# Kernel optimization log

Measured on AMD Instinct MI355X. Metric: run time of the kernel, lower is better.

Reference implementation:

```python
import jax, jax.numpy as jnp
import numpy as np
from jax import lax
import math

B, C, H, W = 2, 128, 128, 256
K = 3
KK = K * K
AUX = C + 5

def conv2d(x, w, b, pad):
    out = lax.conv_general_dilated(x, w, (1, 1), [(pad, pad), (pad, pad)],
                                   dimension_numbers=('NCHW', 'OIHW', 'NCHW'))
    return out + b[None, :, None, None]

def erp_coord(h, w):
    xs = jnp.linspace(-math.pi, math.pi, w)
    ys = jnp.linspace(-math.pi / 2, math.pi / 2, h)
    theta = jnp.broadcast_to(xs[None, :], (h, w))
    phi = jnp.broadcast_to(ys[:, None], (h, w))
    return jnp.stack([jnp.sin(theta), jnp.cos(theta), jnp.sin(phi), jnp.cos(phi)], 0)[None]

def freq_energy(x, h, w):
    mag = jnp.abs(jnp.fft.rfft2(x, norm='ortho')).mean(1, keepdims=True)
    # bilinear resize (align_corners=False, half-pixel) to (h, w)
    return jax.image.resize(mag, (x.shape[0], 1, h, w), method='linear', antialias=False)

def deform_sample(x, offset):
    # x: (b,c,H,W); offset: (b, 2*KK, H, W)
    b, c, h, w = x.shape
    off = offset.reshape(b, KK, 2, h, w)
    xx = jnp.arange(w, dtype=x.dtype)[None, None, None, :]
    yy = jnp.arange(h, dtype=x.dtype)[None, None, :, None]
    # align_corners=True normalize/unnormalize cancels exactly
    px = xx + off[:, :, 0]  # (b,KK,h,w)
    py = yy + off[:, :, 1]
    x0 = jnp.floor(px).astype(jnp.int32); x1 = x0 + 1
    y0 = jnp.floor(py).astype(jnp.int32); y1 = y0 + 1
    wx1 = px - x0.astype(x.dtype); wx0 = 1.0 - wx1
    wy1 = py - y0.astype(x.dtype); wy0 = 1.0 - wy1
    flat = x.reshape(b, c, h * w)

    def gather(ix, iy):
        valid = ((ix >= 0) & (ix < w) & (iy >= 0) & (iy < h)).astype(x.dtype)
        idx = jnp.clip(iy, 0, h - 1) * w + jnp.clip(ix, 0, w - 1)  # (b,KK,h,w)
        g = jax.vmap(lambda f, i: f[:, i])(flat, idx)  # (b,c,KK,h,w)
        return g * valid[:, None]

    out = (gather(x0, y0) * (wx0 * wy0)[:, None]
           + gather(x1, y0) * (wx1 * wy0)[:, None]
           + gather(x0, y1) * (wx0 * wy1)[:, None]
           + gather(x1, y1) * (wx1 * wy1)[:, None])
    return out.reshape(b, c * KK, h, w)

def setup_inputs() -> dict:
    key = jax.random.key(0)
    ks = jax.random.split(key, 12)
    s = lambda *sh: 1.0 / np.sqrt(np.prod(sh[1:]))
    def unif(k, *sh):
        return jax.random.uniform(k, sh, jnp.float32, -s(*sh), s(*sh))
    return {
        'x': jax.random.normal(ks[0], (B, C, H, W), jnp.float32),
        'offset_w': unif(ks[1], 2 * KK, AUX, 3, 3),
        'offset_b': jnp.zeros((2 * KK,), jnp.float32),
        'gate_w1': unif(ks[2], AUX // 2, AUX, 3, 3),
        'gate_b1': jnp.zeros((AUX // 2,), jnp.float32),
        'gate_w2': unif(ks[3], 1, AUX // 2, 1, 1),
        'gate_b2': jnp.zeros((1,), jnp.float32),
        'base_w': unif(ks[4], C, C, K, K),
        'base_b': jnp.zeros((C,), jnp.float32),
        'def_w': jax.random.normal(ks[5], (C, C, K, K), jnp.float32) * s(C, C, K, K),
        'def_b': jnp.zeros((C,), jnp.float32),
    }

def reference(x, offset_w, offset_b, gate_w1, gate_b1, gate_w2, gate_b2,
              base_w, base_b, def_w, def_b):
    b, c, h, w = x.shape
    coord = jnp.broadcast_to(erp_coord(h, w), (b, 4, h, w)).astype(x.dtype)
    fe = freq_energy(x, h, w)
    aux = jnp.concatenate([x, coord, fe], 1)
    offset = conv2d(aux, offset_w, offset_b, 1)
    g = jax.nn.relu(conv2d(aux, gate_w1, gate_b1, 1))
    gate = jax.nn.sigmoid(conv2d(g, gate_w2, gate_b2, 0))
    y_base = conv2d(x, base_w, base_b, K // 2)
    sampled = deform_sample(x, offset)  # (b, c*KK, h, w)
    y_def = conv2d(sampled, def_w.reshape(c, c * KK, 1, 1), def_b, 0)
    return (1.0 - gate) * y_base + gate * y_def
```

## Files before the change

kernel.cpp:

```cpp
#include <hip/hip_runtime.h>
#include <hip/hip_bf16.h>

#define BB 2
#define CC 128
#define HH 128
#define WW 256
#define HWs (HH*WW)
#define PI_F 3.14159265358979323846f

typedef __attribute__((ext_vector_type(8))) short bf16x8;
typedef __attribute__((ext_vector_type(8))) unsigned short u16x8;
typedef __attribute__((ext_vector_type(4))) float f32x4;
typedef __attribute__((ext_vector_type(2))) float f32x2;

__device__ __forceinline__ ushort f2bf(float f) {
  uint u = __float_as_uint(f);
  u = (u + 0x7fffu + ((u >> 16) & 1u)) >> 16;
  return (ushort)u;
}
__device__ __forceinline__ float bf2f(ushort u) {
  return __uint_as_float(((uint)u) << 16);
}
__device__ __forceinline__ uint comb4(uint u0, uint u1, uint u2, uint u3,
                                      f32x2 g0, f32x2 g1, f32x2 g2, f32x2 g3) {
  f32x2 a0 = (f32x2){__uint_as_float(u0 << 16), __uint_as_float(u0 & 0xffff0000u)};
  f32x2 a1 = (f32x2){__uint_as_float(u1 << 16), __uint_as_float(u1 & 0xffff0000u)};
  f32x2 a2 = (f32x2){__uint_as_float(u2 << 16), __uint_as_float(u2 & 0xffff0000u)};
  f32x2 a3 = (f32x2){__uint_as_float(u3 << 16), __uint_as_float(u3 & 0xffff0000u)};
  f32x2 s = a0 * g0 + a1 * g1 + a2 * g2 + a3 * g3;
  uint ua = __float_as_uint(s.x) + 0x8000u;
  uint ub = __float_as_uint(s.y) + 0x8000u;
  return (ua >> 16) | (ub & 0xffff0000u);
}

__global__ __launch_bounds__(256) void prep_kernel(
    const float* __restrict__ bw, const float* __restrict__ dw,
    const float* __restrict__ ow, const float* __restrict__ gw,
    const float* __restrict__ x,
    ushort* __restrict__ apkF, ushort* __restrict__ apkA,
    ushort* __restrict__ a1, ushort* __restrict__ a2,
    ushort* __restrict__ xt) {
  __shared__ ushort sT[64][128];
  int bid = blockIdx.x;
  int tid = threadIdx.x;
  if (bid >= 284) {
    int blk = bid - 284;
    int wt = blk & 3, h = (blk >> 2) & 127, b = blk >> 9;
    int t = tid;
    const float* xb = x + ((size_t)b * CC * HH + h) * WW;
    ushort* ob = xt + (((size_t)b * HH + h) * WW) * 128;
    {
      int w = t & 63;
      int sw = (w & 7) << 3;
#pragma unroll
      for (int it = 0; it < 4; ++it) {
        int oct = (t >> 6) + it * 4;
        u16x8 v;
#pragma unroll
        for (int j = 0; j < 8; ++j)
          v[j] = f2bf(xb[(size_t)(oct * 8 + j) * HWs + wt * 64 + w]);
        *(u16x8*)&sT[w][(oct << 3) ^ sw] = v;
      }
    }
    __syncthreads();
#pragma unroll
    for (int it = 0; it < 4; ++it) {
      int u = t + it * 256;
      int w = u >> 4, oct = u & 15;
      u16x8 v = *(const u16x8*)&sT[w][(oct << 3) ^ ((w & 7) << 3)];
      *(u16x8*)&ob[(size_t)(wt * 64 + w) * 128 + oct * 8] = v;
    }
    return;
  }
  if (bid < 144) {
    int gid = bid * 256 + tid;
    int lane = gid & 63;
    int kf = (gid >> 6) & 3;
    int mf = (gid >> 8) & 7;
    int chunk = gid >> 11;
    int part = chunk >= 9;
    int tap = part ? chunk - 9 : chunk;
    int m = mf * 16 + (lane & 15);
    int cb = kf * 32 + ((lane >> 4) << 3);
    const float* src = part ? dw : bw;
    ushort* dst = apkF + (size_t)gid * 8;
#pragma unroll
    for (int j = 0; j < 8; ++j)
      dst[j] = f2bf(src[(size_t)m * 1152 + (size_t)(cb + j) * 9 + tap]);
  } else if (bid < 212) {
    int gid = (bid - 144) * 256 + tid;
    if (gid >= 17280) return;
    int lane = gid & 63;
    int kf = (gid >> 6) % 5;
    int mf = (gid / 320) % 6;
    int tap = gid / 1920;
    int m = mf * 16 + (lane & 15);
    int cb = kf * 32 + ((lane >> 4) << 3);
#pragma unroll
    for (int j = 0; j < 8; ++j) {
      int c = cb + j;
      float v = 0.f;
      if (c < 133) {
        if (m < 18) v = ow[(size_t)m * 1197 + c * 9 + tap];
        else if (m < 84) v = gw[(size_t)(m - 18) * 1197 + c * 9 + tap];
      }
      apkA[(size_t)gid * 8 + j] = f2bf(v);
    }
  } else {
    int gid = (bid - 212) * 256 + tid;
    if (gid < 10240) {
      int lane = gid & 63, kf = (gid >> 6) & 7, mf = gid >> 9;
      int m = mf * 16 + (lane & 15);
      int kk0 = kf * 32 + ((lane >> 4) << 3);
#pragma unroll
      for (int j = 0; j < 8; ++j) {
        int kk = kk0 + j;
        float v = 0.f;
        if (m < 129)      { int tt = (m * kk) & 255;         v =  cosf(tt * (PI_F / 128.f)); }
        else if (m < 258) { int tt = ((m - 129) * kk) & 255; v = -sinf(tt * (PI_F / 128.f)); }
        a1[(size_t)gid * 8 + j] = f2bf(v);
      }
    } else if (gid < 18432) {
      int q = gid - 10240;
      int lane = q & 63, kf = (q >> 6) & 7, mf = q >> 9;
      int m = mf * 16 + (lane & 15);
      int g = m & 127;
      int kk0 = kf * 32 + ((lane >> 4) << 3);
#pragma unroll
      for (int j = 0; j < 8; ++j) {
        int kk = kk0 + j;
        int h2 = kk & 127;
        int tt = (g * h2) & 127;
        float ang = tt * (PI_F / 64.f);
        float v = (m < 128) ? ((kk < 128) ? cosf(ang) : sinf(ang))
                            : ((kk < 128) ? -sinf(ang) : cosf(ang));
        a2[(size_t)q * 8 + j] = f2bf(v);
      }
    }
  }
}

__global__ __launch_bounds__(256) void dft1_kernel(const float* __restrict__ x,
    const ushort* __restrict__ a1pk, ushort* __restrict__ F1) {
  int bid = blockIdx.x;
  int bc = bid >> 1, nh = bid & 1;
  int t = threadIdx.x, lane = t & 63, wv = t >> 6;
  int q8 = (lane >> 4) << 3, rq = (lane >> 4) << 2;
  const bf16x8* APK = (const bf16x8*)a1pk;
  ushort* f1b = F1 + (size_t)bc * 36864;
  f32x4 acc[5][4];
#pragma unroll
  for (int i = 0; i < 5; ++i)
#pragma unroll
    for (int n = 0; n < 4; ++n) acc[i][n] = (f32x4){0.f, 0.f, 0.f, 0.f};
  for (int kf = 0; kf < 8; ++kf) {
    bf16x8 av[5];
#pragma unroll
    for (int i = 0; i < 5; ++i)
      av[i] = APK[(size_t)((wv * 5 + i) * 8 + kf) * 64 + lane];
#pragma unroll
    for (int n2 = 0; n2 < 4; ++n2) {
      int nf = nh * 4 + n2;
      int hh = nf * 16 + (lane & 15);
      const float* xp = x + (((size_t)bc * HH + hh) << 8) + kf * 32 + q8;
      float4 xa = *(const float4*)xp;
      float4 xb4 = *(const float4*)(xp + 4);
      bf16x8 bv;
      bv[0] = (short)f2bf(xa.x); bv[1] = (short)f2bf(xa.y);
      bv[2] = (short)f2bf(xa.z); bv[3] = (short)f2bf(xa.w);
      bv[4] = (short)f2bf(xb4.x); bv[5] = (short)f2bf(xb4.y);
      bv[6] = (short)f2bf(xb4.z); bv[7] = (short)f2bf(xb4.w);
#pragma unroll
      for (int i = 0; i < 5; ++i)
        acc[i][n2] = __builtin_amdgcn_mfma_f32_16x16x32_bf16(av[i], bv, acc[i][n2], 0, 0, 0);
    }
  }
#pragma unroll
  for (int n2 = 0; n2 < 4; ++n2) {
    int hh = (nh * 4 + n2) * 16 + (lane & 15);
#pragma unroll
    for (int i = 0; i < 5; ++i) {
#pragma unroll
      for (int r = 0; r < 4; ++r) {
        int m = (wv * 5 + i) * 16 + rq + r;
        if (m < 258) {
          int sel = m >= 129;
          int k = sel ? m - 129 : m;
          f1b[(size_t)k * 256 + sel * 128 + hh] = f2bf(acc[i][n2][r]);
        }
      }
    }
  }
}

__global__ __launch_bounds__(256) void dft2_kernel(const ushort* __restrict__ F1,
    const ushort* __restrict__ a2pk, float* __restrict__ magbuf) {
  int bid = blockIdx.x;
  int bc = bid / 3, ng = bid % 3;
  int t = threadIdx.x, lane = t & 63, wv = t >> 6;
  int q8 = (lane >> 4) << 3, rq = (lane >> 4) << 2;
  const bf16x8* APK = (const bf16x8*)a2pk;
  const ushort* f1b = F1 + (size_t)bc * 36864;
  float* mb = magbuf + (size_t)bc * 18432;
  f32x4 acc[4][3];
#pragma unroll
  for (int i = 0; i < 4; ++i)
#pragma unroll
    for (int n = 0; n < 3; ++n) acc[i][n] = (f32x4){0.f, 0.f, 0.f, 0.f};
  for (int kf = 0; kf < 8; ++kf) {
    bf16x8 av[4];
#pragma unroll
    for (int i = 0; i < 4; ++i) {
      int mf = (i < 2) ? (2 * wv + i) : (2 * wv + (i - 2) + 8);
      av[i] = APK[(size_t)(mf * 8 + kf) * 64 + lane];
    }
#pragma unroll
    for (int n2 = 0; n2 < 3; ++n2) {
      int nf = ng * 3 + n2;
      int krow = nf * 16 + (lane & 15);
      bf16x8 bv = *(const bf16x8*)&f1b[(size_t)krow * 256 + kf * 32 + q8];
#pragma unroll
      for (int i = 0; i < 4; ++i)
        acc[i][n2] = __builtin_amdgcn_mfma_f32_16x16x32_bf16(av[i], bv, acc[i][n2], 0, 0, 0);
    }
  }
#pragma unroll
  for (int n2 = 0; n2 < 3; ++n2) {
    int k = (ng * 3 + n2) * 16 + (lane & 15);
    if (k < 129) {
#pragma unroll
      for (int pr = 0; pr < 2; ++pr) {
#pragma unroll
        for (int r = 0; r < 4; ++r) {
          int g = (2 * wv + pr) * 16 + rq + r;
          float vr = acc[pr][n2][r], vi = acc[pr + 2][n2][r];
          mb[(size_t)g * 144 + k] = sqrtf(vr * vr + vi * vi);
        }
      }
    }
  }
}

__global__ __launch_bounds__(256) void fe_reduce_kernel(const float* __restrict__ magbuf,
    float* __restrict__ fe) {
  int bid = blockIdx.x;
  int i = (bid >> 3) * 256 + threadIdx.x;
  int cq = bid & 7;
  if (i >= 36864) return;
  int k = i % 144;
  int gb = i / 144;
  int g = gb & 127, b = gb >> 7;
  if (k >= 129) return;
  const float* mp = magbuf + (size_t)b * 128 * 18432 + (size_t)g * 144 + k
                  + (size_t)cq * 16 * 18432;
  float s = 0.f;
#pragma unroll
  for (int c = 0; c < 16; ++c) s += mp[(size_t)c * 18432];
  atomicAdd(&fe[((size_t)b * 128 + g) * 129 + k],
            s * (1.0f / (181.01933598375618f * 128.0f)));
}

__global__ __launch_bounds__(256) void aux_conv_kernel(
    const ushort* __restrict__ xt, const float* __restrict__ fe,
    const ushort* __restrict__ apk,
    const float* __restrict__ offset_b, const float* __restrict__ gate_b1,
    const float* __restrict__ w2, const float* __restrict__ b2,
    float* __restrict__ offs, float* __restrict__ gate) {
  __shared__ ushort Win3[3 * 68 * 64];
  __shared__ ushort coordS[204 * 8];
  __shared__ float gldP[64][8];
  int t = threadIdx.x;
  int bid = blockIdx.x;
  int lin = (bid & 7) * 128 + (bid >> 3);
  int bz = lin >> 9;
  int rest = lin & 511;
  int h = rest >> 2, w0 = (rest & 3) << 6;
  int lane = t & 63, wid = t >> 6;
  int wm = wid >> 1, wn = wid & 1;
  int l15 = lane & 15, lg = lane >> 4;
  int rq = lg << 2;
  const bf16x8* APK = (const bf16x8*)apk;
  const ushort* xtb = xt + (size_t)bz * 4194304;
  const bf16x8 zvb = (bf16x8){0, 0, 0, 0, 0, 0, 0, 0};

  if (t < 204) {
    int r = t / 68, c = t - r * 68;
    int gy = h - 1 + r, gx = w0 - 2 + c;
    u16x8 v = (u16x8){0, 0, 0, 0, 0, 0, 0, 0};
    if ((unsigned)gy < 128u && (unsigned)gx < 256u) {
      float th = -PI_F + (float)gx * (2.0f * PI_F / 255.0f);
      float ph = -0.5f * PI_F + (float)gy * (PI_F / 127.0f);
      float sxc = ((float)gx + 0.5f) * (129.0f / 256.0f) - 0.5f;
      float fx = floorf(sxc);
      int x0 = (int)fx;
      float fr = sxc - fx;
      int x1 = min(x0 + 1, 128);
      x0 = max(x0, 0);
      const float* fb = fe + ((size_t)bz * 128 + gy) * 129;
      float fv = fb[x0] * (1.f - fr) + fb[x1] * fr;
      v[0] = f2bf(sinf(th)); v[1] = f2bf(cosf(th));
      v[2] = f2bf(sinf(ph)); v[3] = f2bf(cosf(ph));
      v[4] = f2bf(fv);
    }
    *(u16x8*)&coordS[t * 8] = v;
  }

  f32x4 acc[3][2];
#pragma unroll
  for (int i = 0; i < 3; ++i) {
    acc[i][0] = (f32x4){0.f, 0.f, 0.f, 0.f};
    acc[i][1] = (f32x4){0.f, 0.f, 0.f, 0.f};
  }
  int p0 = wn * 32 + l15, p1 = p0 + 16;

  for (int half = 0; half < 2; ++half) {
    if (half) __syncthreads();
    for (int it = 0; it < 7; ++it) {
      int u = it * 256 + t;
      if (u < 1632) {
        int s = u & 7;
        int c = (u >> 3) % 68;
        int r = u / 544;
        int gy = h - 1 + r, gx = w0 - 2 + c;
        u16x8 v = (u16x8){0, 0, 0, 0, 0, 0, 0, 0};
        if ((unsigned)gy < 128u && (unsigned)gx < 256u)
          v = *(const u16x8*)&xtb[((((size_t)gy << 8) + gx) << 7) + (half << 6) + (s << 3)];
        *(u16x8*)&Win3[((r * 68 + c) << 6) + ((s ^ (c & 7)) << 3)] = v;
      }
    }
    __syncthreads();

    for (int tap = 0; tap < 9; ++tap) {
      int ky = tap / 3 - 1, kx = tap % 3 - 1;
      int rr = ky + 1;
      int c0 = p0 + kx + 2, c1 = p1 + kx + 2;
      int nkf = half ? 3 : 2;
      for (int kfi = 0; kfi < nkf; ++kfi) {
        bf16x8 b0, b1;
        int kf;
        if (kfi < 2) {
          kf = half * 2 + kfi;
          int s = kfi * 4 + lg;
          b0 = *(const bf16x8*)&Win3[((rr * 68 + c0) << 6) + ((s ^ (c0 & 7)) << 3)];
          b1 = *(const bf16x8*)&Win3[((rr * 68 + c1) << 6) + ((s ^ (c1 & 7)) << 3)];
        } else {
          kf = 4;
          b0 = (lg == 0) ? *(const bf16x8*)&coordS[(rr * 68 + c0) * 8] : zvb;
          b1 = (lg == 0) ? *(const bf16x8*)&coordS[(rr * 68 + c1) * 8] : zvb;
        }
        int fb = (tap * 6 + wm * 3) * 5 + kf;
#pragma unroll
        for (int mfi = 0; mfi < 3; ++mfi) {
          bf16x8 av = APK[(size_t)(fb + mfi * 5) * 64 + lane];
          acc[mfi][0] = __builtin_amdgcn_mfma_f32_16x16x32_bf16(av, b0, acc[mfi][0], 0, 0, 0);
          acc[mfi][1] = __builtin_amdgcn_mfma_f32_16x16x32_bf16(av, b1, acc[mfi][1], 0, 0, 0);
        }
      }
    }
  }

  float gp[2] = {0.f, 0.f};
#pragma unroll
  for (int nf = 0; nf < 2; ++nf) {
    int p = wn * 32 + nf * 16 + l15;
    int w = w0 + p;
#pragma unroll
    for (int mfi = 0; mfi < 3; ++mfi) {
#pragma unroll
      for (int r = 0; r < 4; ++r) {
        int oc = wm * 48 + mfi * 16 + rq + r;
        float v = acc[mfi][nf][r];
        if (oc < 18) {
          offs[((size_t)bz * 18 + oc) * HWs + h * WW + w] = v + offset_b[oc];
        } else if (oc < 84) {
          gp[nf] += w2[oc - 18] * fmaxf(v + gate_b1[oc - 18], 0.f);
        }
      }
    }
  }
  gldP[p0][wm * 4 + lg] = gp[0];
  gldP[p1][wm * 4 + lg] = gp[1];
  __syncthreads();
  if (t < 64) {
    float s = b2[0];
#pragma unroll
    for (int i = 0; i < 8; ++i) s += gldP[t][i];
    gate[(size_t)bz * HWs + h * WW + w0 + t] = 1.f / (1.f + expf(-s));
  }
}

__global__ __launch_bounds__(256) void fused_out_kernel(
    const ushort* __restrict__ xt, const float* __restrict__ offsp,
    const ushort* __restrict__ apk,
    const float* __restrict__ base_b, const float* __restrict__ def_b,
    const float* __restrict__ gate, float* __restrict__ out) {
  __shared__ ushort Win[4 * 68 * 64];
  __shared__ ushort Bt[2][64][64];
  __shared__ float gvS[64];
  __shared__ float bbS[128], bdS[128];
  int t = threadIdx.x;
  int bid = blockIdx.x;
  int lin = (bid & 7) * 128 + (bid >> 3);
  int bz = lin >> 9;
  int rest = lin & 511;
  int h = rest >> 2, w0 = (rest & 3) << 6;
  int lane = t & 63, wv = t >> 6;
  int l15 = lane & 15, lg = lane >> 4;
  int rq = lg << 2;
  const ushort* xtb = xt + (size_t)bz * 4194304;
  const bf16x8* APK = (const bf16x8*)apk;
  const u16x8 zv = (u16x8){0, 0, 0, 0, 0, 0, 0, 0};

  if (t < 64) gvS[t] = gate[(size_t)bz * HWs + h * WW + w0 + t];
  else if (t < 192) {
    int c = t - 64;
    bbS[c] = base_b[c];
    bdS[c] = def_b[c];
  }

  int p = t & 63, o4 = t >> 6;
  int mw = w0 + p;
  float oxr[9], oyr[9];
#pragma unroll
  for (int d = 0; d < 9; ++d) {
    oxr[d] = offsp[((size_t)bz * 18 + 2 * d) * HWs + h * WW + mw];
    oyr[d] = offsp[((size_t)bz * 18 + 2 * d + 1) * HWs + h * WW + mw];
  }

  f32x4 accB[2][4], accD[2][4];
#pragma unroll
  for (int mi = 0; mi < 2; ++mi)
#pragma unroll
    for (int nf = 0; nf < 4; ++nf) {
      accB[mi][nf] = (f32x4){0.f, 0.f, 0.f, 0.f};
      accD[mi][nf] = (f32x4){0.f, 0.f, 0.f, 0.f};
    }

  for (int half = 0; half < 2; ++half) {
#pragma unroll
    for (int it = 0; it < 9; ++it) {
      int u = it * 256 + t;
      if (u < 2176) {
        int s = u & 7;
        int c = (u >> 3) % 68;
        int r = u / 544;
        int gy = h - 1 + r, gx = w0 - 2 + c;
        u16x8 v = zv;
        if ((unsigned)gy < 128u && (unsigned)gx < 256u)
          v = *(const u16x8*)&xtb[((((size_t)gy << 8) + gx) << 7) + (half << 6) + (s << 3)];
        *(u16x8*)&Win[((r * 68 + c) << 6) + ((s ^ (c & 7)) << 3)] = v;
      }
    }
    __syncthreads();

    auto stage = [&](int nb, int d) {
      float px = (float)mw + oxr[d], py = (float)h + oyr[d];
      float fx = floorf(px), fy = floorf(py);
      int x0 = (int)fx, y0 = (int)fy;
      float wx1 = px - fx, wy1 = py - fy;
      float wx0 = 1.f - wx1, wy0 = 1.f - wy1;
      int x1 = x0 + 1, y1 = y0 + 1;
      bool vx0 = (unsigned)x0 < 256u, vx1 = (unsigned)x1 < 256u;
      bool vy0 = (unsigned)y0 < 128u, vy1 = (unsigned)y1 < 128u;
      float g0 = (vx0 && vy0) ? wx0 * wy0 : 0.f;
      float g1 = (vx1 && vy0) ? wx1 * wy0 : 0.f;
      float g2 = (vx0 && vy1) ? wx0 * wy1 : 0.f;
      float g3 = (vx1 && vy1) ? wx1 * wy1 : 0.f;
      f32x2 G0 = (f32x2){g0, g0}, G1 = (f32x2){g1, g1};
      f32x2 G2 = (f32x2){g2, g2}, G3 = (f32x2){g3, g3};
      int cx0 = min(max(x0, 0), 255), cx1 = min(max(x1, 0), 255);
      int cy0 = min(max(y0, 0), 127), cy1 = min(max(y1, 0), 127);
      int rx0 = cx0 - w0 + 2, rx1 = cx1 - w0 + 2;
      int ry0 = cy0 - h + 1,  ry1 = cy1 - h + 1;
      bool i00 = ((unsigned)ry0 < 4u) && ((unsigned)rx0 < 68u);
      bool i01 = ((unsigned)ry0 < 4u) && ((unsigned)rx1 < 68u);
      bool i10 = ((unsigned)ry1 < 4u) && ((unsigned)rx0 < 68u);
      bool i11 = ((unsigned)ry1 < 4u) && ((unsigned)rx1 < 68u);
      int wb0 = ((ry0 * 68 + rx0) << 6) ^ ((rx0 & 7) << 3);
      int wb1 = ((ry0 * 68 + rx1) << 6) ^ ((rx1 & 7) << 3);
      int wb2 = ((ry1 * 68 + rx0) << 6) ^ ((rx0 & 7) << 3);
      int wb3 = ((ry1 * 68 + rx1) << 6) ^ ((rx1 & 7) << 3);
      int gb0 = (((cy0 << 8) + cx0) << 7) + (half << 6);
      int gb1 = (((cy0 << 8) + cx1) << 7) + (half << 6);
      int gb2 = (((cy1 << 8) + cx0) << 7) + (half << 6);
      int gb3 = (((cy1 << 8) + cx1) << 7) + (half << 6);
#pragma unroll
      for (int oo = 0; oo < 2; ++oo) {
        int o = o4 + oo * 4;
        int o8 = o << 3;
        uint4 c0, c1, c2, c3;
        if (i00) c0 = *(const uint4*)&Win[wb0 ^ o8];
        else     c0 = *(const uint4*)&xtb[gb0 + o8];
        if (i01) c1 = *(const uint4*)&Win[wb1 ^ o8];
        else     c1 = *(const uint4*)&xtb[gb1 + o8];
        if (i10) c2 = *(const uint4*)&Win[wb2 ^ o8];
        else     c2 = *(const uint4*)&xtb[gb2 + o8];
        if (i11) c3 = *(const uint4*)&Win[wb3 ^ o8];
        else     c3 = *(const uint4*)&xtb[gb3 + o8];
        uint4 r;
        r.x = comb4(c0.x, c1.x, c2.x, c3.x, G0, G1, G2, G3);
        r.y = comb4(c0.y, c1.y, c2.y, c3.y, G0, G1, G2, G3);
        r.z = comb4(c0.z, c1.z, c2.z, c3.z, G0, G1, G2, G3);
        r.w = comb4(c0.w, c1.w, c2.w, c3.w, G0, G1, G2, G3);
        *(uint4*)&Bt[nb][p][(o ^ (p & 7)) << 3] = r;
      }
    };

    stage(0, 0);
    __syncthreads();

    int buf = 0;
    for (int d = 0; d < 9; ++d) {
      int ky = d / 3 - 1, kx = d % 3 - 1;
      int ryB = ky + 1;
#pragma unroll
      for (int kfi = 0; kfi < 2; ++kfi) {
        int kff = half * 2 + kfi;
        int segk = kfi * 4 + lg;
        bf16x8 aB0 = APK[(size_t)((d * 8 + wv) * 4 + kff) * 64 + lane];
        bf16x8 aB1 = APK[(size_t)((d * 8 + wv + 4) * 4 + kff) * 64 + lane];
        bf16x8 aD0 = APK[(size_t)(((9 + d) * 8 + wv) * 4 + kff) * 64 + lane];
        bf16x8 aD1 = APK[(size_t)(((9 + d) * 8 + wv + 4) * 4 + kff) * 64 + lane];
#pragma unroll
        for (int nf = 0; nf < 4; ++nf) {
          int pix = nf * 16 + l15;
          int cxr = pix + kx + 2;
          bf16x8 bB = *(const bf16x8*)&Win[((ryB * 68 + cxr) << 6) + ((segk ^ (cxr & 7)) << 3)];
          bf16x8 bD = *(const bf16x8*)&Bt[buf][pix][(segk ^ (pix & 7)) << 3];
          accB[0][nf] = __builtin_amdgcn_mfma_f32_16x16x32_bf16(aB0, bB, accB[0][nf], 0, 0, 0);
          accB[1][nf] = __builtin_amdgcn_mfma_f32_16x16x32_bf16(aB1, bB, accB[1][nf], 0, 0, 0);
          accD[0][nf] = __builtin_amdgcn_mfma_f32_16x16x32_bf16(aD0, bD, accD[0][nf], 0, 0, 0);
          accD[1][nf] = __builtin_amdgcn_mfma_f32_16x16x32_bf16(aD1, bD, accD[1][nf], 0, 0, 0);
        }
      }
      if (d < 8) stage(buf ^ 1, d + 1);
      __syncthreads();
      buf ^= 1;
    }
    if (half == 0) __syncthreads();
  }

#pragma unroll
  for (int nf = 0; nf < 4; ++nf) {
    int pix = nf * 16 + l15;
    float gv = gvS[pix], go = 1.f - gv;
    int w = w0 + pix;
#pragma unroll
    for (int mi = 0; mi < 2; ++mi) {
      int mf = wv + mi * 4;
#pragma unroll
      for (int r = 0; r < 4; ++r) {
        int oc = mf * 16 + rq + r;
        out[(((size_t)bz * CC + oc) << 15) + h * WW + w] =
            go * (accB[mi][nf][r] + bbS[oc]) + gv * (accD[mi][nf][r] + bdS[oc]);
      }
    }
  }
}

extern "C" void kernel_launch(void* const* d_in, const int* in_sizes, int n_in,
                              void* d_out, int out_size, void* d_ws, size_t ws_size,
                              hipStream_t stream) {
  const float* x        = (const float*)d_in[0];
  const float* offset_w = (const float*)d_in[1];
  const float* offset_b = (const float*)d_in[2];
  const float* gate_w1  = (const float*)d_in[3];
  const float* gate_b1  = (const float*)d_in[4];
  const float* gate_w2  = (const float*)d_in[5];
  const float* gate_b2  = (const float*)d_in[6];
  const float* base_w   = (const float*)d_in[7];
  const float* base_b   = (const float*)d_in[8];
  const float* def_w    = (const float*)d_in[9];
  const float* def_b    = (const float*)d_in[10];
  float* out = (float*)d_out;
  float* ws  = (float*)d_ws;

  float* offsb   = ws;
  float* gatebuf = offsb + 1179648;
  float* fe      = gatebuf + 65536;
  float* magbuf  = fe + 33024;
  ushort* xt     = (ushort*)(magbuf + 4718592);
  ushort* F1     = xt + 16777216;
  ushort* a1pk   = F1 + 9437184;
  ushort* a2pk   = a1pk + 81920;
  ushort* apkF   = a2pk + 65536;
  ushort* apkA   = apkF + 294912;

  hipMemsetAsync(fe, 0, 33024 * sizeof(float), stream);
  prep_kernel<<<1308, 256, 0, stream>>>(base_w, def_w, offset_w, gate_w1, x,
                                        apkF, apkA, a1pk, a2pk, xt);

  dft1_kernel<<<512, 256, 0, stream>>>(x, a1pk, F1);
  dft2_kernel<<<768, 256, 0, stream>>>(F1, a2pk, magbuf);
  fe_reduce_kernel<<<1152, 256, 0, stream>>>(magbuf, fe);

  aux_conv_kernel<<<1024, 256, 0, stream>>>(xt, fe, apkA, offset_b, gate_b1,
                                            gate_w2, gate_b2, offsb, gatebuf);

  fused_out_kernel<<<1024, 256, 0, stream>>>(xt, offsb, apkF, base_b, def_b,
                                             gatebuf, out);
}
```

Baseline: 195.5 us.

## Fuse aux offset/gate conv with base and deformable conv into one kernel

```diff
diff --git a/kernel.cpp b/kernel.cpp
--- a/kernel.cpp
+++ b/kernel.cpp
@@ -260,33 +260,43 @@
             s * (1.0f / (181.01933598375618f * 128.0f)));
 }
 
-__global__ __launch_bounds__(256) void aux_conv_kernel(
+__global__ __launch_bounds__(256) void fused_all_kernel(
     const ushort* __restrict__ xt, const float* __restrict__ fe,
-    const ushort* __restrict__ apk,
+    const ushort* __restrict__ apkF, const ushort* __restrict__ apkA,
     const float* __restrict__ offset_b, const float* __restrict__ gate_b1,
     const float* __restrict__ w2, const float* __restrict__ b2,
-    float* __restrict__ offs, float* __restrict__ gate) {
-  __shared__ ushort Win3[3 * 68 * 64];
-  __shared__ ushort coordS[204 * 8];
-  __shared__ float gldP[64][8];
+    const float* __restrict__ base_b, const float* __restrict__ def_b,
+    float* __restrict__ out) {
+  __shared__ ushort Win[4 * 68 * 64];
+  __shared__ __align__(16) char Uarena[8192];
+  __shared__ float offS[9][2][64];
+  __shared__ float gvS[64];
+  __shared__ float bbS[128], bdS[128];
+  ushort* Bt = (ushort*)Uarena;
+  ushort* coordS = (ushort*)Uarena;
+  float (*gldP)[8] = (float(*)[8])(Uarena + 3264);
+
   int t = threadIdx.x;
   int bid = blockIdx.x;
   int lin = (bid & 7) * 128 + (bid >> 3);
   int bz = lin >> 9;
   int rest = lin & 511;
   int h = rest >> 2, w0 = (rest & 3) << 6;
-  int lane = t & 63, wid = t >> 6;
-  int wm = wid >> 1, wn = wid & 1;
+  int lane = t & 63, wv = t >> 6;
+  int wm = wv >> 1, wn = wv & 1;
   int l15 = lane & 15, lg = lane >> 4;
   int rq = lg << 2;
-  const bf16x8* APK = (const bf16x8*)apk;
   const ushort* xtb = xt + (size_t)bz * 4194304;
+  const bf16x8* APKF = (const bf16x8*)apkF;
+  const bf16x8* APKA = (const bf16x8*)apkA;
+  const u16x8 zv = (u16x8){0, 0, 0, 0, 0, 0, 0, 0};
   const bf16x8 zvb = (bf16x8){0, 0, 0, 0, 0, 0, 0, 0};
 
+  if (t < 128) { bbS[t] = base_b[t]; bdS[t] = def_b[t]; }
   if (t < 204) {
     int r = t / 68, c = t - r * 68;
     int gy = h - 1 + r, gx = w0 - 2 + c;
-    u16x8 v = (u16x8){0, 0, 0, 0, 0, 0, 0, 0};
+    u16x8 v = zv;
     if ((unsigned)gy < 128u && (unsigned)gx < 256u) {
       float th = -PI_F + (float)gx * (2.0f * PI_F / 255.0f);
       float ph = -0.5f * PI_F + (float)gy * (PI_F / 127.0f);
@@ -305,139 +315,7 @@
     *(u16x8*)&coordS[t * 8] = v;
   }
 
-  f32x4 acc[3][2];
-#pragma unroll
-  for (int i = 0; i < 3; ++i) {
-    acc[i][0] = (f32x4){0.f, 0.f, 0.f, 0.f};
-    acc[i][1] = (f32x4){0.f, 0.f, 0.f, 0.f};
-  }
-  int p0 = wn * 32 + l15, p1 = p0 + 16;
-
-  for (int half = 0; half < 2; ++half) {
-    if (half) __syncthreads();
-    for (int it = 0; it < 7; ++it) {
-      int u = it * 256 + t;
-      if (u < 1632) {
-        int s = u & 7;
-        int c = (u >> 3) % 68;
-        int r = u / 544;
-        int gy = h - 1 + r, gx = w0 - 2 + c;
-        u16x8 v = (u16x8){0, 0, 0, 0, 0, 0, 0, 0};
-        if ((unsigned)gy < 128u && (unsigned)gx < 256u)
-          v = *(const u16x8*)&xtb[((((size_t)gy << 8) + gx) << 7) + (half << 6) + (s << 3)];
-        *(u16x8*)&Win3[((r * 68 + c) << 6) + ((s ^ (c & 7)) << 3)] = v;
-      }
-    }
-    __syncthreads();
-
-    for (int tap = 0; tap < 9; ++tap) {
-      int ky = tap / 3 - 1, kx = tap % 3 - 1;
-      int rr = ky + 1;
-      int c0 = p0 + kx + 2, c1 = p1 + kx + 2;
-      int nkf = half ? 3 : 2;
-      for (int kfi = 0; kfi < nkf; ++kfi) {
-        bf16x8 b0, b1;
-        int kf;
-        if (kfi < 2) {
-          kf = half * 2 + kfi;
-          int s = kfi * 4 + lg;
-          b0 = *(const bf16x8*)&Win3[((rr * 68 + c0) << 6) + ((s ^ (c0 & 7)) << 3)];
-          b1 = *(const bf16x8*)&Win3[((rr * 68 + c1) << 6) + ((s ^ (c1 & 7)) << 3)];
-        } else {
-          kf = 4;
-          b0 = (lg == 0) ? *(const bf16x8*)&coordS[(rr * 68 + c0) * 8] : zvb;
-          b1 = (lg == 0) ? *(const bf16x8*)&coordS[(rr * 68 + c1) * 8] : zvb;
-        }
-        int fb = (tap * 6 + wm * 3) * 5 + kf;
-#pragma unroll
-        for (int mfi = 0; mfi < 3; ++mfi) {
-          bf16x8 av = APK[(size_t)(fb + mfi * 5) * 64 + lane];
-          acc[mfi][0] = __builtin_amdgcn_mfma_f32_16x16x32_bf16(av, b0, acc[mfi][0], 0, 0, 0);
-          acc[mfi][1] = __builtin_amdgcn_mfma_f32_16x16x32_bf16(av, b1, acc[mfi][1], 0, 0, 0);
-        }
-      }
-    }
-  }
-
-  float gp[2] = {0.f, 0.f};
-#pragma unroll
-  for (int nf = 0; nf < 2; ++nf) {
-    int p = wn * 32 + nf * 16 + l15;
-    int w = w0 + p;
-#pragma unroll
-    for (int mfi = 0; mfi < 3; ++mfi) {
-#pragma unroll
-      for (int r = 0; r < 4; ++r) {
-        int oc = wm * 48 + mfi * 16 + rq + r;
-        float v = acc[mfi][nf][r];
-        if (oc < 18) {
-          offs[((size_t)bz * 18 + oc) * HWs + h * WW + w] = v + offset_b[oc];
-        } else if (oc < 84) {
-          gp[nf] += w2[oc - 18] * fmaxf(v + gate_b1[oc - 18], 0.f);
-        }
-      }
-    }
-  }
-  gldP[p0][wm * 4 + lg] = gp[0];
-  gldP[p1][wm * 4 + lg] = gp[1];
-  __syncthreads();
-  if (t < 64) {
-    float s = b2[0];
-#pragma unroll
-    for (int i = 0; i < 8; ++i) s += gldP[t][i];
-    gate[(size_t)bz * HWs + h * WW + w0 + t] = 1.f / (1.f + expf(-s));
-  }
-}
-
-__global__ __launch_bounds__(256) void fused_out_kernel(
-    const ushort* __restrict__ xt, const float* __restrict__ offsp,
-    const ushort* __restrict__ apk,
-    const float* __restrict__ base_b, const float* __restrict__ def_b,
-    const float* __restrict__ gate, float* __restrict__ out) {
-  __shared__ ushort Win[4 * 68 * 64];
-  __shared__ ushort Bt[2][64][64];
-  __shared__ float gvS[64];
-  __shared__ float bbS[128], bdS[128];
-  int t = threadIdx.x;
-  int bid = blockIdx.x;
-  int lin = (bid & 7) * 128 + (bid >> 3);
-  int bz = lin >> 9;
-  int rest = lin & 511;
-  int h = rest >> 2, w0 = (rest & 3) << 6;
-  int lane = t & 63, wv = t >> 6;
-  int l15 = lane & 15, lg = lane >> 4;
-  int rq = lg << 2;
-  const ushort* xtb = xt + (size_t)bz * 4194304;
-  const bf16x8* APK = (const bf16x8*)apk;
-  const u16x8 zv = (u16x8){0, 0, 0, 0, 0, 0, 0, 0};
-
-  if (t < 64) gvS[t] = gate[(size_t)bz * HWs + h * WW + w0 + t];
-  else if (t < 192) {
-    int c = t - 64;
-    bbS[c] = base_b[c];
-    bdS[c] = def_b[c];
-  }
-
-  int p = t & 63, o4 = t >> 6;
-  int mw = w0 + p;
-  float oxr[9], oyr[9];
-#pragma unroll
-  for (int d = 0; d < 9; ++d) {
-    oxr[d] = offsp[((size_t)bz * 18 + 2 * d) * HWs + h * WW + mw];
-    oyr[d] = offsp[((size_t)bz * 18 + 2 * d + 1) * HWs + h * WW + mw];
-  }
-
-  f32x4 accB[2][4], accD[2][4];
-#pragma unroll
-  for (int mi = 0; mi < 2; ++mi)
-#pragma unroll
-    for (int nf = 0; nf < 4; ++nf) {
-      accB[mi][nf] = (f32x4){0.f, 0.f, 0.f, 0.f};
-      accD[mi][nf] = (f32x4){0.f, 0.f, 0.f, 0.f};
-    }
-
-  for (int half = 0; half < 2; ++half) {
-#pragma unroll
+  auto load_win = [&](int half) {
     for (int it = 0; it < 9; ++it) {
       int u = it * 256 + t;
       if (u < 2176) {
@@ -451,94 +329,191 @@
         *(u16x8*)&Win[((r * 68 + c) << 6) + ((s ^ (c & 7)) << 3)] = v;
       }
     }
-    __syncthreads();
-
-    auto stage = [&](int nb, int d) {
-      float px = (float)mw + oxr[d], py = (float)h + oyr[d];
-      float fx = floorf(px), fy = floorf(py);
-      int x0 = (int)fx, y0 = (int)fy;
-      float wx1 = px - fx, wy1 = py - fy;
-      float wx0 = 1.f - wx1, wy0 = 1.f - wy1;
-      int x1 = x0 + 1, y1 = y0 + 1;
-      bool vx0 = (unsigned)x0 < 256u, vx1 = (unsigned)x1 < 256u;
-      bool vy0 = (unsigned)y0 < 128u, vy1 = (unsigned)y1 < 128u;
-      float g0 = (vx0 && vy0) ? wx0 * wy0 : 0.f;
-      float g1 = (vx1 && vy0) ? wx1 * wy0 : 0.f;
-      float g2 = (vx0 && vy1) ? wx0 * wy1 : 0.f;
-      float g3 = (vx1 && vy1) ? wx1 * wy1 : 0.f;
-      f32x2 G0 = (f32x2){g0, g0}, G1 = (f32x2){g1, g1};
-      f32x2 G2 = (f32x2){g2, g2}, G3 = (f32x2){g3, g3};
-      int cx0 = min(max(x0, 0), 255), cx1 = min(max(x1, 0), 255);
-      int cy0 = min(max(y0, 0), 127), cy1 = min(max(y1, 0), 127);
-      int rx0 = cx0 - w0 + 2, rx1 = cx1 - w0 + 2;
-      int ry0 = cy0 - h + 1,  ry1 = cy1 - h + 1;
-      bool i00 = ((unsigned)ry0 < 4u) && ((unsigned)rx0 < 68u);
-      bool i01 = ((unsigned)ry0 < 4u) && ((unsigned)rx1 < 68u);
-      bool i10 = ((unsigned)ry1 < 4u) && ((unsigned)rx0 < 68u);
-      bool i11 = ((unsigned)ry1 < 4u) && ((unsigned)rx1 < 68u);
-      int wb0 = ((ry0 * 68 + rx0) << 6) ^ ((rx0 & 7) << 3);
-      int wb1 = ((ry0 * 68 + rx1) << 6) ^ ((rx1 & 7) << 3);
-      int wb2 = ((ry1 * 68 + rx0) << 6) ^ ((rx0 & 7) << 3);
-      int wb3 = ((ry1 * 68 + rx1) << 6) ^ ((rx1 & 7) << 3);
-      int gb0 = (((cy0 << 8) + cx0) << 7) + (half << 6);
-      int gb1 = (((cy0 << 8) + cx1) << 7) + (half << 6);
-      int gb2 = (((cy1 << 8) + cx0) << 7) + (half << 6);
-      int gb3 = (((cy1 << 8) + cx1) << 7) + (half << 6);
-#pragma unroll
-      for (int oo = 0; oo < 2; ++oo) {
-        int o = o4 + oo * 4;
-        int o8 = o << 3;
-        uint4 c0, c1, c2, c3;
-        if (i00) c0 = *(const uint4*)&Win[wb0 ^ o8];
-        else     c0 = *(const uint4*)&xtb[gb0 + o8];
-        if (i01) c1 = *(const uint4*)&Win[wb1 ^ o8];
-        else     c1 = *(const uint4*)&xtb[gb1 + o8];
-        if (i10) c2 = *(const uint4*)&Win[wb2 ^ o8];
-        else     c2 = *(const uint4*)&xtb[gb2 + o8];
-        if (i11) c3 = *(const uint4*)&Win[wb3 ^ o8];
-        else     c3 = *(const uint4*)&xtb[gb3 + o8];
-        uint4 r;
-        r.x = comb4(c0.x, c1.x, c2.x, c3.x, G0, G1, G2, G3);
-        r.y = comb4(c0.y, c1.y, c2.y, c3.y, G0, G1, G2, G3);
-        r.z = comb4(c0.z, c1.z, c2.z, c3.z, G0, G1, G2, G3);
-        r.w = comb4(c0.w, c1.w, c2.w, c3.w, G0, G1, G2, G3);
-        *(uint4*)&Bt[nb][p][(o ^ (p & 7)) << 3] = r;
-      }
-    };
-
-    stage(0, 0);
-    __syncthreads();
-
-    int buf = 0;
-    for (int d = 0; d < 9; ++d) {
-      int ky = d / 3 - 1, kx = d % 3 - 1;
-      int ryB = ky + 1;
-#pragma unroll
+  };
+
+  f32x4 accA[3][2];
+  f32x4 accB[2][4], accD[2][4];
+#pragma unroll
+  for (int i = 0; i < 3; ++i) {
+    accA[i][0] = (f32x4){0.f, 0.f, 0.f, 0.f};
+    accA[i][1] = (f32x4){0.f, 0.f, 0.f, 0.f};
+  }
+#pragma unroll
+  for (int mi = 0; mi < 2; ++mi)
+#pragma unroll
+    for (int nf = 0; nf < 4; ++nf) {
+      accB[mi][nf] = (f32x4){0.f, 0.f, 0.f, 0.f};
+      accD[mi][nf] = (f32x4){0.f, 0.f, 0.f, 0.f};
+    }
+  int p0a = wn * 32 + l15, p1a = p0a + 16;
+
+  auto aux_base = [&](int half) {
+    for (int tap = 0; tap < 9; ++tap) {
+      int ky = tap / 3 - 1, kx = tap % 3 - 1;
+      int rr = ky + 1;
+      int c0 = p0a + kx + 2, c1 = p1a + kx + 2;
+      int nkf = half ? 3 : 2;
+      for (int kfi = 0; kfi < nkf; ++kfi) {
+        bf16x8 b0, b1;
+        int kf;
+        if (kfi < 2) {
+          kf = half * 2 + kfi;
+          int s = kfi * 4 + lg;
+          b0 = *(const bf16x8*)&Win[((rr * 68 + c0) << 6) + ((s ^ (c0 & 7)) << 3)];
+          b1 = *(const bf16x8*)&Win[((rr * 68 + c1) << 6) + ((s ^ (c1 & 7)) << 3)];
+        } else {
+          kf = 4;
+          b0 = (lg == 0) ? *(const bf16x8*)&coordS[(rr * 68 + c0) * 8] : zvb;
+          b1 = (lg == 0) ? *(const bf16x8*)&coordS[(rr * 68 + c1) * 8] : zvb;
+        }
+        int fb = (tap * 6 + wm * 3) * 5 + kf;
+#pragma unroll
+        for (int mfi = 0; mfi < 3; ++mfi) {
+          bf16x8 av = APKA[(size_t)(fb + mfi * 5) * 64 + lane];
+          accA[mfi][0] = __builtin_amdgcn_mfma_f32_16x16x32_bf16(av, b0, accA[mfi][0], 0, 0, 0);
+          accA[mfi][1] = __builtin_amdgcn_mfma_f32_16x16x32_bf16(av, b1, accA[mfi][1], 0, 0, 0);
+        }
+      }
       for (int kfi = 0; kfi < 2; ++kfi) {
         int kff = half * 2 + kfi;
         int segk = kfi * 4 + lg;
-        bf16x8 aB0 = APK[(size_t)((d * 8 + wv) * 4 + kff) * 64 + lane];
-        bf16x8 aB1 = APK[(size_t)((d * 8 + wv + 4) * 4 + kff) * 64 + lane];
-        bf16x8 aD0 = APK[(size_t)(((9 + d) * 8 + wv) * 4 + kff) * 64 + lane];
-        bf16x8 aD1 = APK[(size_t)(((9 + d) * 8 + wv + 4) * 4 + kff) * 64 + lane];
+        bf16x8 aB0 = APKF[(size_t)((tap * 8 + wv) * 4 + kff) * 64 + lane];
+        bf16x8 aB1 = APKF[(size_t)((tap * 8 + wv + 4) * 4 + kff) * 64 + lane];
 #pragma unroll
         for (int nf = 0; nf < 4; ++nf) {
           int pix = nf * 16 + l15;
           int cxr = pix + kx + 2;
-          bf16x8 bB = *(const bf16x8*)&Win[((ryB * 68 + cxr) << 6) + ((segk ^ (cxr & 7)) << 3)];
-          bf16x8 bD = *(const bf16x8*)&Bt[buf][pix][(segk ^ (pix & 7)) << 3];
+          bf16x8 bB = *(const bf16x8*)&Win[((rr * 68 + cxr) << 6) + ((segk ^ (cxr & 7)) << 3)];
           accB[0][nf] = __builtin_amdgcn_mfma_f32_16x16x32_bf16(aB0, bB, accB[0][nf], 0, 0, 0);
           accB[1][nf] = __builtin_amdgcn_mfma_f32_16x16x32_bf16(aB1, bB, accB[1][nf], 0, 0, 0);
+        }
+      }
+    }
+  };
+
+  int p = t & 63, o4 = t >> 6;
+  int mw = w0 + p;
+  auto stage = [&](int d, int half) {
+    float px = (float)mw + offS[d][0][p], py = (float)h + offS[d][1][p];
+    float fx = floorf(px), fy = floorf(py);
+    int x0 = (int)fx, y0 = (int)fy;
+    float wx1 = px - fx, wy1 = py - fy;
+    float wx0 = 1.f - wx1, wy0 = 1.f - wy1;
+    int x1 = x0 + 1, y1 = y0 + 1;
+    bool vx0 = (unsigned)x0 < 256u, vx1 = (unsigned)x1 < 256u;
+    bool vy0 = (unsigned)y0 < 128u, vy1 = (unsigned)y1 < 128u;
+    float g0 = (vx0 && vy0) ? wx0 * wy0 : 0.f;
+    float g1 = (vx1 && vy0) ? wx1 * wy0 : 0.f;
+    float g2 = (vx0 && vy1) ? wx0 * wy1 : 0.f;
+    float g3 = (vx1 && vy1) ? wx1 * wy1 : 0.f;
+    f32x2 G0 = (f32x2){g0, g0}, G1 = (f32x2){g1, g1};
+    f32x2 G2 = (f32x2){g2, g2}, G3 = (f32x2){g3, g3};
+    int cx0 = min(max(x0, 0), 255), cx1 = min(max(x1, 0), 255);
+    int cy0 = min(max(y0, 0), 127), cy1 = min(max(y1, 0), 127);
+    int rx0 = cx0 - w0 + 2, rx1 = cx1 - w0 + 2;
+    int ry0 = cy0 - h + 1,  ry1 = cy1 - h + 1;
+    bool i00 = ((unsigned)ry0 < 4u) && ((unsigned)rx0 < 68u);
+    bool i01 = ((unsigned)ry0 < 4u) && ((unsigned)rx1 < 68u);
+    bool i10 = ((unsigned)ry1 < 4u) && ((unsigned)rx0 < 68u);
+    bool i11 = ((unsigned)ry1 < 4u) && ((unsigned)rx1 < 68u);
+    int wb0 = ((ry0 * 68 + rx0) << 6) ^ ((rx0 & 7) << 3);
+    int wb1 = ((ry0 * 68 + rx1) << 6) ^ ((rx1 & 7) << 3);
+    int wb2 = ((ry1 * 68 + rx0) << 6) ^ ((rx0 & 7) << 3);
+    int wb3 = ((ry1 * 68 + rx1) << 6) ^ ((rx1 & 7) << 3);
+    int gb0 = (((cy0 << 8) + cx0) << 7) + (half << 6);
+    int gb1 = (((cy0 << 8) + cx1) << 7) + (half << 6);
+    int gb2 = (((cy1 << 8) + cx0) << 7) + (half << 6);
+    int gb3 = (((cy1 << 8) + cx1) << 7) + (half << 6);
+#pragma unroll
+    for (int oo = 0; oo < 2; ++oo) {
+      int o = o4 + oo * 4;
+      int o8 = o << 3;
+      uint4 c0, c1, c2, c3;
+      if (i00) c0 = *(const uint4*)&Win[wb0 ^ o8];
+      else     c0 = *(const uint4*)&xtb[gb0 + o8];
+      if (i01) c1 = *(const uint4*)&Win[wb1 ^ o8];
+      else     c1 = *(const uint4*)&xtb[gb1 + o8];
+      if (i10) c2 = *(const uint4*)&Win[wb2 ^ o8];
+      else     c2 = *(const uint4*)&xtb[gb2 + o8];
+      if (i11) c3 = *(const uint4*)&Win[wb3 ^ o8];
+      else     c3 = *(const uint4*)&xtb[gb3 + o8];
+      uint4 r;
+      r.x = comb4(c0.x, c1.x, c2.x, c3.x, G0, G1, G2, G3);
+      r.y = comb4(c0.y, c1.y, c2.y, c3.y, G0, G1, G2, G3);
+      r.z = comb4(c0.z, c1.z, c2.z, c3.z, G0, G1, G2, G3);
+      r.w = comb4(c0.w, c1.w, c2.w, c3.w, G0, G1, G2, G3);
+      *(uint4*)&Bt[(p << 6) + ((o ^ (p & 7)) << 3)] = r;
+    }
+  };
+
+  auto deform_half = [&](int half) {
+    stage(0, half);
+    __syncthreads();
+    for (int d = 0; d < 9; ++d) {
+      for (int kfi = 0; kfi < 2; ++kfi) {
+        int kff = half * 2 + kfi;
+        int segk = kfi * 4 + lg;
+        bf16x8 aD0 = APKF[(size_t)(((9 + d) * 8 + wv) * 4 + kff) * 64 + lane];
+        bf16x8 aD1 = APKF[(size_t)(((9 + d) * 8 + wv + 4) * 4 + kff) * 64 + lane];
+#pragma unroll
+        for (int nf = 0; nf < 4; ++nf) {
+          int pix = nf * 16 + l15;
+          bf16x8 bD = *(const bf16x8*)&Bt[(pix << 6) + ((segk ^ (pix & 7)) << 3)];
           accD[0][nf] = __builtin_amdgcn_mfma_f32_16x16x32_bf16(aD0, bD, accD[0][nf], 0, 0, 0);
           accD[1][nf] = __builtin_amdgcn_mfma_f32_16x16x32_bf16(aD1, bD, accD[1][nf], 0, 0, 0);
         }
       }
-      if (d < 8) stage(buf ^ 1, d + 1);
       __syncthreads();
-      buf ^= 1;
-    }
-    if (half == 0) __syncthreads();
-  }
+      if (d < 8) {
+        stage(d + 1, half);
+        __syncthreads();
+      }
+    }
+  };
+
+  __syncthreads();
+  load_win(0);
+  __syncthreads();
+  aux_base(0);
+  __syncthreads();
+  load_win(1);
+  __syncthreads();
+  aux_base(1);
+  {
+    float gp[2] = {0.f, 0.f};
+#pragma unroll
+    for (int nf = 0; nf < 2; ++nf) {
+      int pp = wn * 32 + nf * 16 + l15;
+#pragma unroll
+      for (int mfi = 0; mfi < 3; ++mfi) {
+#pragma unroll
+        for (int r = 0; r < 4; ++r) {
+          int oc = wm * 48 + mfi * 16 + rq + r;
+          float v = accA[mfi][nf][r];
+          if (oc < 18) {
+            offS[oc >> 1][oc & 1][pp] = v + offset_b[oc];
+          } else if (oc < 84) {
+            gp[nf] += w2[oc - 18] * fmaxf(v + gate_b1[oc - 18], 0.f);
+          }
+        }
+      }
+    }
+    __syncthreads();
+    gldP[p0a][wm * 4 + lg] = gp[0];
+    gldP[p1a][wm * 4 + lg] = gp[1];
+    __syncthreads();
+    if (t < 64) {
+      float s = b2[0];
+#pragma unroll
+      for (int i = 0; i < 8; ++i) s += gldP[t][i];
+      gvS[t] = 1.f / (1.f + expf(-s));
+    }
+    __syncthreads();
+  }
+  deform_half(1);
+  load_win(0);
+  __syncthreads();
+  deform_half(0);
 
 #pragma unroll
   for (int nf = 0; nf < 4; ++nf) {
@@ -575,9 +550,7 @@
   float* out = (float*)d_out;
   float* ws  = (float*)d_ws;
 
-  float* offsb   = ws;
-  float* gatebuf = offsb + 1179648;
-  float* fe      = gatebuf + 65536;
+  float* fe      = ws;
   float* magbuf  = fe + 33024;
   ushort* xt     = (ushort*)(magbuf + 4718592);
   ushort* F1     = xt + 16777216;
@@ -594,9 +567,7 @@
   dft2_kernel<<<768, 256, 0, stream>>>(F1, a2pk, magbuf);
   fe_reduce_kernel<<<1152, 256, 0, stream>>>(magbuf, fe);
 
-  aux_conv_kernel<<<1024, 256, 0, stream>>>(xt, fe, apkA, offset_b, gate_b1,
-                                            gate_w2, gate_b2, offsb, gatebuf);
-
-  fused_out_kernel<<<1024, 256, 0, stream>>>(xt, offsb, apkF, base_b, def_b,
-                                             gatebuf, out);
-}
+  fused_all_kernel<<<1024, 256, 0, stream>>>(xt, fe, apkF, apkA,
+                                             offset_b, gate_b1, gate_w2, gate_b2,
+                                             base_b, def_b, out);
+}
```

New measurement: 202.1 us. 1.03x slower.
